# Kernel optimization log

Measured on AMD Instinct MI355X. Metric: run time of the kernel, lower is better.

Reference implementation:

```python
import jax, jax.numpy as jnp
import numpy as np

HIDDEN = 1024
HEADS = 16
HEAD_DIM = HIDDEN // HEADS
SCALE = HEAD_DIM ** -0.5


def setup_inputs() -> dict:
    key = jax.random.key(0)
    kx, kw, ko = jax.random.split(key, 3)
    x = jax.random.normal(kx, (2, 2048, HIDDEN), dtype=jnp.float32)
    # nn.Linear(hidden, 3*hidden, bias=False): weight shape [3*hidden, hidden]
    w_qkv = jax.random.normal(kw, (3 * HIDDEN, HIDDEN), dtype=jnp.float32) * (HIDDEN ** -0.5)
    w_out = jax.random.normal(ko, (HIDDEN, HIDDEN), dtype=jnp.float32) * (HIDDEN ** -0.5)
    return {"x": x, "w_qkv": w_qkv, "w_out": w_out}


def reference(x, w_qkv, w_out):
    b, s, d = x.shape
    qkv = jnp.einsum('bsd,ed->bse', x, w_qkv)  # [b,s,3d]
    q, k, v = jnp.split(qkv, 3, axis=-1)
    def heads(t):
        return t.reshape(b, s, HEADS, HEAD_DIM).transpose(0, 2, 1, 3)  # [b,h,s,hd]
    q, k, v = heads(q), heads(k), heads(v)
    scores = jnp.einsum('bhqd,bhkd->bhqk', q, k) * SCALE
    attn = jax.nn.softmax(scores, axis=-1)
    out = jnp.einsum('bhqk,bhkd->bhqd', attn, v)
    out = out.transpose(0, 2, 1, 3).reshape(b, s, d)
    return jnp.einsum('bsd,ed->bse', out, w_out)
```

## Files before the change

### kernel.cpp

```cpp
#include <hip/hip_runtime.h>
#include <hip/hip_bf16.h>
#include <stdint.h>

typedef __bf16 bf16;
typedef __bf16 bf16x8 __attribute__((ext_vector_type(8)));
typedef float f32x4 __attribute__((ext_vector_type(4)));

#define HIDDEN 1024
#define HEADS  16
#define HD     64
#define SEQ    2048
#define BATCH  2
#define NTOK   (BATCH*SEQ)
#define E3     (3*HIDDEN)

#define QSCALE (0.125f * 1.44269504088896f)

#if __has_builtin(__builtin_amdgcn_exp2f)
#define EXP2(x) __builtin_amdgcn_exp2f(x)
#else
#define EXP2(x) __expf((x) * 0.69314718055995f)
#endif

static __device__ __forceinline__ uint32_t pkbf(float a, float b) {
  union { bf16 h[2]; uint32_t u; } x;
  x.h[0] = (bf16)a; x.h[1] = (bf16)b;
  return x.u;
}

__global__ __launch_bounds__(256) void k_convert(
    const float* __restrict__ x, const float* __restrict__ wqkv, const float* __restrict__ wout,
    bf16* __restrict__ xb, bf16* __restrict__ wqkvb, bf16* __restrict__ woutb)
{
  const int NX = NTOK*HIDDEN/4, NW = E3*HIDDEN/4;
  int i = blockIdx.x*256 + threadIdx.x;
  const float4* s; bf16* d; int o;
  if (i < NX)            { s=(const float4*)x;    d=xb;    o=i; }
  else if (i < NX+NW)    { s=(const float4*)wqkv; d=wqkvb; o=i-NX; }
  else                   { s=(const float4*)wout; d=woutb; o=i-NX-NW; }
  float4 v = s[o];
  union { bf16 b[4]; uint2 u; } p;
  p.b[0]=(bf16)v.x; p.b[1]=(bf16)v.y; p.b[2]=(bf16)v.z; p.b[3]=(bf16)v.w;
  *(uint2*)(d + (size_t)o*4) = p.u;
}

template<int EPI, int BM>
__global__ __launch_bounds__(256) void k_gemm(
    const bf16* __restrict__ A, const bf16* __restrict__ B,
    bf16* __restrict__ Oq, bf16* __restrict__ Ok, bf16* __restrict__ Ov,
    float* __restrict__ Of, int M, int N, int K, int nbn)
{
  constexpr int MI = BM/32;
  __shared__ bf16 As[BM*32];
  __shared__ bf16 Bs[128*32];
  const int t = threadIdx.x;
  const int lane = t & 63;
  const int w = t >> 6;
  const int g = lane >> 4;
  const int l15 = lane & 15;
  const int wm = (w >> 1) * (BM/2), wn = (w & 1) * 64;
  const int bm = blockIdx.x / nbn, bn = blockIdx.x % nbn;
  const int brow = bm*BM, bcol = bn*128;

  f32x4 acc[MI][4];
  #pragma unroll
  for (int mi=0;mi<MI;mi++)
    #pragma unroll
    for (int ni=0;ni<4;ni++)
      #pragma unroll
      for (int r=0;r<4;r++) acc[mi][ni][r] = 0.f;

  const int nk = K >> 5;
  for (int kt = 0; kt < nk; ++kt) {
    if constexpr (BM == 128) {
      int ch = w*128 + lane;
      const bf16* ga = A + (size_t)(brow + (ch>>2))*K + kt*32 + (ch&3)*8;
      __builtin_amdgcn_global_load_lds((const uint32_t*)ga, (uint32_t*)(As + (w*128)*8), 16, 0, 0);
      int ch2 = ch + 64;
      const bf16* ga2 = A + (size_t)(brow + (ch2>>2))*K + kt*32 + (ch2&3)*8;
      __builtin_amdgcn_global_load_lds((const uint32_t*)ga2, (uint32_t*)(As + (w*128+64)*8), 16, 0, 0);
    } else {
      int ch = w*64 + lane;
      const bf16* ga = A + (size_t)(brow + (ch>>2))*K + kt*32 + (ch&3)*8;
      __builtin_amdgcn_global_load_lds((const uint32_t*)ga, (uint32_t*)(As + (w*64)*8), 16, 0, 0);
    }
    {
      int ch = w*128 + lane;
      const bf16* gb = B + (size_t)(bcol + (ch>>2))*K + kt*32 + (ch&3)*8;
      __builtin_amdgcn_global_load_lds((const uint32_t*)gb, (uint32_t*)(Bs + (w*128)*8), 16, 0, 0);
      int ch2 = ch + 64;
      const bf16* gb2 = B + (size_t)(bcol + (ch2>>2))*K + kt*32 + (ch2&3)*8;
      __builtin_amdgcn_global_load_lds((const uint32_t*)gb2, (uint32_t*)(Bs + (w*128+64)*8), 16, 0, 0);
    }
    __syncthreads();
    bf16x8 af[MI], bfr[4];
    #pragma unroll
    for (int mi=0;mi<MI;mi++) af[mi]  = *(const bf16x8*)(As + (wm + mi*16 + l15)*32 + g*8);
    #pragma unroll
    for (int ni=0;ni<4;ni++) bfr[ni] = *(const bf16x8*)(Bs + (wn + ni*16 + l15)*32 + g*8);
    #pragma unroll
    for (int mi=0;mi<MI;mi++)
      #pragma unroll
      for (int ni=0;ni<4;ni++)
        acc[mi][ni] = __builtin_amdgcn_mfma_f32_16x16x32_bf16(af[mi], bfr[ni], acc[mi][ni], 0, 0, 0);
    __syncthreads();
  }

  #pragma unroll
  for (int mi=0;mi<MI;mi++) {
    #pragma unroll
    for (int ni=0;ni<4;ni++) {
      #pragma unroll
      for (int r=0;r<4;r++) {
        float val = acc[mi][ni][r];
        int m = brow + wm + mi*16 + 4*g + r;
        int e = bcol + wn + ni*16 + l15;
        if (EPI == 0) {
          int part = e >> 10, we = e & 1023;
          int hh = we >> 6, dd = we & 63;
          int b = m >> 11, sb = m & 2047;
          size_t idx = (((size_t)b*HEADS + hh)*SEQ + sb)*HD + dd;
          if (part == 0)      Oq[idx] = (bf16)(val * QSCALE);
          else if (part == 1) Ok[idx] = (bf16)val;
          else                Ov[idx] = (bf16)val;
        } else {
          Of[(size_t)m*HIDDEN + e] = val;
        }
      }
    }
  }
}

__global__ __launch_bounds__(256, 2) void k_attn(
    const bf16* __restrict__ Qg, const bf16* __restrict__ Kg, const bf16* __restrict__ Vg,
    bf16* __restrict__ Og)
{
  __shared__ bf16 Kl[64*64];
  __shared__ bf16 Vt[64*64];
  const int t = threadIdx.x;
  const int lane = t & 63;
  const int w = t >> 6;
  const int g = lane >> 4;
  const int q = lane & 15;
  const int bh = blockIdx.x >> 4;
  const int qb = blockIdx.x & 15;
  const int q0 = qb*128 + w*32;
  const size_t bhS = (size_t)bh * SEQ * HD;

  bf16x8 qf[2][2];
  #pragma unroll
  for (int qs=0;qs<2;qs++) {
    const bf16* qrow = Qg + bhS + (size_t)(q0 + 16*qs + q)*HD + 8*g;
    qf[qs][0] = *(const bf16x8*)(qrow);
    qf[qs][1] = *(const bf16x8*)(qrow + 32);
  }

  f32x4 ot[2][4];
  #pragma unroll
  for (int qs=0;qs<2;qs++)
    #pragma unroll
    for (int df=0;df<4;df++)
      #pragma unroll
      for (int r=0;r<4;r++) ot[qs][df][r] = 0.f;
  float mrun0 = -3.0e38f, mrun1 = -3.0e38f, lrun0 = 0.f, lrun1 = 0.f;

  const int kr0 = t >> 3, kp0 = t & 7;
  const int kv0 = (t & 31)*2;
  const int dd0 = (t >> 5)*8;
  const int kvf0 = kv0 >> 4, gv = (kv0 >> 2) & 3, rv = kv0 & 3;
  const int pos0 = 32*(kvf0 >> 1) + 8*gv + 4*(kvf0 & 1) + rv;

  auto loadK = [&](int it, uint4& a, uint4& b) {
    const bf16* p0 = Kg + bhS + (size_t)(it*64 + kr0)*HD + kp0*8;
    a = *(const uint4*)p0;
    b = *(const uint4*)(p0 + 32*HD);
  };
  auto writeK = [&](uint4 a, uint4 b) {
    int sw = (kp0 ^ (kr0 & 7)) * 16;
    *(uint4*)((char*)Kl + kr0*128 + sw) = a;
    *(uint4*)((char*)Kl + (kr0+32)*128 + sw) = b;
  };
  auto loadV = [&](int it, uint4& a, uint4& b) {
    const bf16* vg = Vg + bhS + (size_t)(it*64 + kv0)*HD + dd0;
    a = *(const uint4*)vg;
    b = *(const uint4*)(vg + HD);
  };
  auto writeVt = [&](uint4 va, uint4 vb) {
    const uint32_t* pa = (const uint32_t*)&va;
    const uint32_t* pb = (const uint32_t*)&vb;
    #pragma unroll
    for (int jj=0;jj<8;jj++) {
      int dd = dd0 + jj;
      uint32_t pr = __builtin_amdgcn_perm(pb[jj>>1], pa[jj>>1],
                                          (jj&1) ? 0x07060302u : 0x05040100u);
      int byte = (dd*128 + pos0*2) ^ (jj<<4);
      *(uint32_t*)((char*)Vt + byte) = pr;
    }
  };

  uint4 ka, kb, va, vb;
  loadK(0, ka, kb);
  loadV(0, va, vb);

  const int NT = SEQ/64;
  for (int it = 0; it < NT; ++it) {
    __syncthreads();
    writeK(ka, kb);
    writeVt(va, vb);
    __syncthreads();
    if (it+1 < NT) {
      loadK(it+1, ka, kb);
      loadV(it+1, va, vb);
    }

    f32x4 sf[2][4];
    #pragma unroll
    for (int qs=0;qs<2;qs++)
      #pragma unroll
      for (int kvf=0;kvf<4;kvf++)
        #pragma unroll
        for (int r=0;r<4;r++) sf[qs][kvf][r] = 0.f;
    #pragma unroll
    for (int kvf=0;kvf<4;kvf++) {
      int row = 16*kvf + q;
      #pragma unroll
      for (int kc=0;kc<2;kc++) {
        int byte = row*128 + ((16*g + 64*kc) ^ ((row&7)<<4));
        bf16x8 kf = *(const bf16x8*)((const char*)Kl + byte);
        sf[0][kvf] = __builtin_amdgcn_mfma_f32_16x16x32_bf16(kf, qf[0][kc], sf[0][kvf], 0,0,0);
        sf[1][kvf] = __builtin_amdgcn_mfma_f32_16x16x32_bf16(kf, qf[1][kc], sf[1][kvf], 0,0,0);
      }
    }

    float pm0 = -3.0e38f, pm1 = -3.0e38f;
    #pragma unroll
    for (int kvf=0;kvf<4;kvf++)
      #pragma unroll
      for (int r=0;r<4;r++) {
        pm0 = fmaxf(pm0, sf[0][kvf][r]);
        pm1 = fmaxf(pm1, sf[1][kvf][r]);
      }
    pm0 = fmaxf(pm0, __shfl_xor(pm0, 16, 64));
    pm0 = fmaxf(pm0, __shfl_xor(pm0, 32, 64));
    pm1 = fmaxf(pm1, __shfl_xor(pm1, 16, 64));
    pm1 = fmaxf(pm1, __shfl_xor(pm1, 32, 64));

    bool need = (pm0 - mrun0 > 8.f) || (pm1 - mrun1 > 8.f);
    if (__any(need)) {
      float mn0 = fmaxf(mrun0, pm0), mn1 = fmaxf(mrun1, pm1);
      float a0 = EXP2(mrun0 - mn0), a1 = EXP2(mrun1 - mn1);
      lrun0 *= a0; lrun1 *= a1;
      #pragma unroll
      for (int df=0;df<4;df++)
        #pragma unroll
        for (int r=0;r<4;r++) { ot[0][df][r] *= a0; ot[1][df][r] *= a1; }
      mrun0 = mn0; mrun1 = mn1;
    }
    float rs0 = 0.f, rs1 = 0.f;
    #pragma unroll
    for (int kvf=0;kvf<4;kvf++)
      #pragma unroll
      for (int r=0;r<4;r++) {
        float p0 = EXP2(sf[0][kvf][r] - mrun0); sf[0][kvf][r] = p0; rs0 += p0;
        float p1 = EXP2(sf[1][kvf][r] - mrun1); sf[1][kvf][r] = p1; rs1 += p1;
      }
    rs0 += __shfl_xor(rs0, 16, 64); rs0 += __shfl_xor(rs0, 32, 64);
    rs1 += __shfl_xor(rs1, 16, 64); rs1 += __shfl_xor(rs1, 32, 64);
    lrun0 += rs0; lrun1 += rs1;

    uint32_t pk[2][4][2];
    #pragma unroll
    for (int qs=0;qs<2;qs++)
      #pragma unroll
      for (int kvf=0;kvf<4;kvf++) {
        pk[qs][kvf][0] = pkbf(sf[qs][kvf][0], sf[qs][kvf][1]);
        pk[qs][kvf][1] = pkbf(sf[qs][kvf][2], sf[qs][kvf][3]);
      }

    #pragma unroll
    for (int kc=0;kc<2;kc++) {
      union { uint32_t u[4]; bf16x8 v; } pf0, pf1;
      pf0.u[0] = pk[0][2*kc][0]; pf0.u[1] = pk[0][2*kc][1];
      pf0.u[2] = pk[0][2*kc+1][0]; pf0.u[3] = pk[0][2*kc+1][1];
      pf1.u[0] = pk[1][2*kc][0]; pf1.u[1] = pk[1][2*kc][1];
      pf1.u[2] = pk[1][2*kc+1][0]; pf1.u[3] = pk[1][2*kc+1][1];
      #pragma unroll
      for (int df=0;df<4;df++) {
        int row = 16*df + q;
        int byte = row*128 + ((16*g + 64*kc) ^ ((row&7)<<4));
        bf16x8 vf = *(const bf16x8*)((const char*)Vt + byte);
        ot[0][df] = __builtin_amdgcn_mfma_f32_16x16x32_bf16(vf, pf0.v, ot[0][df], 0,0,0);
        ot[1][df] = __builtin_amdgcn_mfma_f32_16x16x32_bf16(vf, pf1.v, ot[1][df], 0,0,0);
      }
    }
  }

  float inv0 = 1.0f / lrun0, inv1 = 1.0f / lrun1;
  int b = bh >> 4, head = bh & 15;
  #pragma unroll
  for (int qs=0;qs<2;qs++) {
    float inv = qs ? inv1 : inv0;
    size_t orow = ((size_t)b*SEQ + q0 + 16*qs + q)*HIDDEN + head*HD;
    #pragma unroll
    for (int df=0;df<4;df++) {
      uint2 pr;
      pr.x = pkbf(ot[qs][df][0]*inv, ot[qs][df][1]*inv);
      pr.y = pkbf(ot[qs][df][2]*inv, ot[qs][df][3]*inv);
      *(uint2*)(Og + orow + 16*df + 4*g) = pr;
    }
  }
}

extern "C" void kernel_launch(void* const* d_in, const int* in_sizes, int n_in,
                              void* d_out, int out_size, void* d_ws, size_t ws_size,
                              hipStream_t stream)
{
  (void)in_sizes; (void)n_in; (void)out_size; (void)ws_size;
  const float* x    = (const float*)d_in[0];
  const float* wqkv = (const float*)d_in[1];
  const float* wout = (const float*)d_in[2];
  float* out = (float*)d_out;
  char* ws = (char*)d_ws;
  bf16* xb    = (bf16*)(ws);
  bf16* wqkvb = (bf16*)(ws + 8388608);
  bf16* woutb = (bf16*)(ws + 14680064);
  bf16* Q     = (bf16*)(ws + 16777216);
  bf16* K     = (bf16*)(ws + 25165824);
  bf16* V     = (bf16*)(ws + 33554432);
  bf16* O     = (bf16*)(ws + 41943040);

  k_convert<<<8192, 256, 0, stream>>>(x, wqkv, wout, xb, wqkvb, woutb);
  k_gemm<0,128><<<32*24, 256, 0, stream>>>(xb, wqkvb, Q, K, V, nullptr, NTOK, E3, HIDDEN, 24);
  k_attn<<<512, 256, 0, stream>>>(Q, K, V, O);
  k_gemm<1,64><<<64*8, 256, 0, stream>>>(O, woutb, nullptr, nullptr, nullptr, out, NTOK, HIDDEN, HIDDEN, 8);
}
```

Baseline: 194.9 us.

## Double-buffer attention K/V tiles with software-pipelined QK/softmax-PV and widen GEMM K-tile

The GEMM now loads 64-wide K slices per iteration into swizzled shared memory, which halves the number of barrier pairs and is meant to avoid LDS bank conflicts. The attention kernel double-buffers its K and V tiles. It interleaves the QK^T of the next tile with the softmax and PV of the previous one, and raises wave priority around the MFMA blocks. This should overlap matrix-core work with softmax math and LDS traffic. The cost is double the LDS footprint and more live registers, which may lower occupancy under launch_bounds(256,2).

```diff
diff --git a/kernel.cpp b/kernel.cpp
--- a/kernel.cpp
+++ b/kernel.cpp
@@ -51,8 +51,8 @@
     float* __restrict__ Of, int M, int N, int K, int nbn)
 {
   constexpr int MI = BM/32;
-  __shared__ bf16 As[BM*32];
-  __shared__ bf16 Bs[128*32];
+  __shared__ bf16 As[BM*64];
+  __shared__ bf16 Bs[128*64];
   const int t = threadIdx.x;
   const int lane = t & 63;
   const int w = t >> 6;
@@ -70,39 +70,44 @@
       #pragma unroll
       for (int r=0;r<4;r++) acc[mi][ni][r] = 0.f;
 
-  const int nk = K >> 5;
+  const int nk = K >> 6;
   for (int kt = 0; kt < nk; ++kt) {
-    if constexpr (BM == 128) {
-      int ch = w*128 + lane;
-      const bf16* ga = A + (size_t)(brow + (ch>>2))*K + kt*32 + (ch&3)*8;
-      __builtin_amdgcn_global_load_lds((const uint32_t*)ga, (uint32_t*)(As + (w*128)*8), 16, 0, 0);
-      int ch2 = ch + 64;
-      const bf16* ga2 = A + (size_t)(brow + (ch2>>2))*K + kt*32 + (ch2&3)*8;
-      __builtin_amdgcn_global_load_lds((const uint32_t*)ga2, (uint32_t*)(As + (w*128+64)*8), 16, 0, 0);
-    } else {
-      int ch = w*64 + lane;
-      const bf16* ga = A + (size_t)(brow + (ch>>2))*K + kt*32 + (ch&3)*8;
-      __builtin_amdgcn_global_load_lds((const uint32_t*)ga, (uint32_t*)(As + (w*64)*8), 16, 0, 0);
-    }
-    {
-      int ch = w*128 + lane;
-      const bf16* gb = B + (size_t)(bcol + (ch>>2))*K + kt*32 + (ch&3)*8;
-      __builtin_amdgcn_global_load_lds((const uint32_t*)gb, (uint32_t*)(Bs + (w*128)*8), 16, 0, 0);
-      int ch2 = ch + 64;
-      const bf16* gb2 = B + (size_t)(bcol + (ch2>>2))*K + kt*32 + (ch2&3)*8;
-      __builtin_amdgcn_global_load_lds((const uint32_t*)gb2, (uint32_t*)(Bs + (w*128+64)*8), 16, 0, 0);
+    #pragma unroll
+    for (int j=0; j<BM/32; j++) {
+      int ch = w*(BM*2) + j*64 + lane;
+      int row = ch>>3, part = ch&7;
+      const bf16* ga = A + (size_t)(brow+row)*K + kt*64 + (part ^ (row&7))*8;
+      __builtin_amdgcn_global_load_lds((const uint32_t*)ga,
+          (uint32_t*)(As + (size_t)(w*(BM*2) + j*64)*8), 16, 0, 0);
+    }
+    #pragma unroll
+    for (int j=0; j<4; j++) {
+      int ch = w*256 + j*64 + lane;
+      int row = ch>>3, part = ch&7;
+      const bf16* gb = B + (size_t)(bcol+row)*K + kt*64 + (part ^ (row&7))*8;
+      __builtin_amdgcn_global_load_lds((const uint32_t*)gb,
+          (uint32_t*)(Bs + (size_t)(w*256 + j*64)*8), 16, 0, 0);
     }
     __syncthreads();
-    bf16x8 af[MI], bfr[4];
-    #pragma unroll
-    for (int mi=0;mi<MI;mi++) af[mi]  = *(const bf16x8*)(As + (wm + mi*16 + l15)*32 + g*8);
-    #pragma unroll
-    for (int ni=0;ni<4;ni++) bfr[ni] = *(const bf16x8*)(Bs + (wn + ni*16 + l15)*32 + g*8);
-    #pragma unroll
-    for (int mi=0;mi<MI;mi++)
-      #pragma unroll
-      for (int ni=0;ni<4;ni++)
-        acc[mi][ni] = __builtin_amdgcn_mfma_f32_16x16x32_bf16(af[mi], bfr[ni], acc[mi][ni], 0, 0, 0);
+    #pragma unroll
+    for (int kc=0; kc<2; kc++) {
+      bf16x8 af[MI], bfr[4];
+      #pragma unroll
+      for (int mi=0;mi<MI;mi++) {
+        int row = wm + mi*16 + l15;
+        af[mi] = *(const bf16x8*)((const char*)As + row*128 + ((kc*64 + g*16) ^ ((row&7)<<4)));
+      }
+      #pragma unroll
+      for (int ni=0;ni<4;ni++) {
+        int row = wn + ni*16 + l15;
+        bfr[ni] = *(const bf16x8*)((const char*)Bs + row*128 + ((kc*64 + g*16) ^ ((row&7)<<4)));
+      }
+      #pragma unroll
+      for (int mi=0;mi<MI;mi++)
+        #pragma unroll
+        for (int ni=0;ni<4;ni++)
+          acc[mi][ni] = __builtin_amdgcn_mfma_f32_16x16x32_bf16(af[mi], bfr[ni], acc[mi][ni], 0, 0, 0);
+    }
     __syncthreads();
   }
 
@@ -135,8 +140,8 @@
     const bf16* __restrict__ Qg, const bf16* __restrict__ Kg, const bf16* __restrict__ Vg,
     bf16* __restrict__ Og)
 {
-  __shared__ bf16 Kl[64*64];
-  __shared__ bf16 Vt[64*64];
+  __shared__ bf16 Kl[2][64*64];
+  __shared__ bf16 Vt[2][64*64];
   const int t = threadIdx.x;
   const int lane = t & 63;
   const int w = t >> 6;
@@ -175,63 +180,54 @@
     a = *(const uint4*)p0;
     b = *(const uint4*)(p0 + 32*HD);
   };
-  auto writeK = [&](uint4 a, uint4 b) {
+  auto writeK = [&](int buf, uint4 a, uint4 b) {
     int sw = (kp0 ^ (kr0 & 7)) * 16;
-    *(uint4*)((char*)Kl + kr0*128 + sw) = a;
-    *(uint4*)((char*)Kl + (kr0+32)*128 + sw) = b;
+    char* base = (char*)&Kl[buf][0];
+    *(uint4*)(base + kr0*128 + sw) = a;
+    *(uint4*)(base + (kr0+32)*128 + sw) = b;
   };
   auto loadV = [&](int it, uint4& a, uint4& b) {
     const bf16* vg = Vg + bhS + (size_t)(it*64 + kv0)*HD + dd0;
     a = *(const uint4*)vg;
     b = *(const uint4*)(vg + HD);
   };
-  auto writeVt = [&](uint4 va, uint4 vb) {
+  auto writeVt = [&](int buf, uint4 va, uint4 vb) {
     const uint32_t* pa = (const uint32_t*)&va;
     const uint32_t* pb = (const uint32_t*)&vb;
+    char* base = (char*)&Vt[buf][0];
     #pragma unroll
     for (int jj=0;jj<8;jj++) {
       int dd = dd0 + jj;
       uint32_t pr = __builtin_amdgcn_perm(pb[jj>>1], pa[jj>>1],
                                           (jj&1) ? 0x07060302u : 0x05040100u);
       int byte = (dd*128 + pos0*2) ^ (jj<<4);
-      *(uint32_t*)((char*)Vt + byte) = pr;
-    }
-  };
-
-  uint4 ka, kb, va, vb;
-  loadK(0, ka, kb);
-  loadV(0, va, vb);
-
-  const int NT = SEQ/64;
-  for (int it = 0; it < NT; ++it) {
-    __syncthreads();
-    writeK(ka, kb);
-    writeVt(va, vb);
-    __syncthreads();
-    if (it+1 < NT) {
-      loadK(it+1, ka, kb);
-      loadV(it+1, va, vb);
-    }
-
-    f32x4 sf[2][4];
+      *(uint32_t*)(base + byte) = pr;
+    }
+  };
+
+  auto doQK = [&](const char* Kbase, f32x4 (&sf)[2][4]) {
     #pragma unroll
     for (int qs=0;qs<2;qs++)
       #pragma unroll
       for (int kvf=0;kvf<4;kvf++)
         #pragma unroll
         for (int r=0;r<4;r++) sf[qs][kvf][r] = 0.f;
+    __builtin_amdgcn_s_setprio(1);
     #pragma unroll
     for (int kvf=0;kvf<4;kvf++) {
       int row = 16*kvf + q;
       #pragma unroll
       for (int kc=0;kc<2;kc++) {
         int byte = row*128 + ((16*g + 64*kc) ^ ((row&7)<<4));
-        bf16x8 kf = *(const bf16x8*)((const char*)Kl + byte);
+        bf16x8 kf = *(const bf16x8*)(Kbase + byte);
         sf[0][kvf] = __builtin_amdgcn_mfma_f32_16x16x32_bf16(kf, qf[0][kc], sf[0][kvf], 0,0,0);
         sf[1][kvf] = __builtin_amdgcn_mfma_f32_16x16x32_bf16(kf, qf[1][kc], sf[1][kvf], 0,0,0);
       }
     }
-
+    __builtin_amdgcn_s_setprio(0);
+  };
+
+  auto doSMPV = [&](const char* Vbase, f32x4 (&sf)[2][4]) {
     float pm0 = -3.0e38f, pm1 = -3.0e38f;
     #pragma unroll
     for (int kvf=0;kvf<4;kvf++)
@@ -277,6 +273,7 @@
         pk[qs][kvf][1] = pkbf(sf[qs][kvf][2], sf[qs][kvf][3]);
       }
 
+    __builtin_amdgcn_s_setprio(1);
     #pragma unroll
     for (int kc=0;kc<2;kc++) {
       union { uint32_t u[4]; bf16x8 v; } pf0, pf1;
@@ -288,12 +285,44 @@
       for (int df=0;df<4;df++) {
         int row = 16*df + q;
         int byte = row*128 + ((16*g + 64*kc) ^ ((row&7)<<4));
-        bf16x8 vf = *(const bf16x8*)((const char*)Vt + byte);
+        bf16x8 vf = *(const bf16x8*)(Vbase + byte);
         ot[0][df] = __builtin_amdgcn_mfma_f32_16x16x32_bf16(vf, pf0.v, ot[0][df], 0,0,0);
         ot[1][df] = __builtin_amdgcn_mfma_f32_16x16x32_bf16(vf, pf1.v, ot[1][df], 0,0,0);
       }
     }
-  }
+    __builtin_amdgcn_s_setprio(0);
+  };
+
+  const char* K0 = (const char*)&Kl[0][0];
+  const char* K1 = (const char*)&Kl[1][0];
+  const char* V0 = (const char*)&Vt[0][0];
+  const char* V1 = (const char*)&Vt[1][0];
+
+  uint4 ka, kb, va, vb;
+  loadK(0, ka, kb); loadV(0, va, vb);
+  writeK(0, ka, kb); writeVt(0, va, vb);
+  __syncthreads();
+  loadK(1, ka, kb); loadV(1, va, vb);
+
+  f32x4 sfA[2][4], sfB[2][4];
+  const int NT = SEQ/64;
+  for (int it = 0; it < NT; it += 2) {
+    doQK(K0, sfA);
+    if (it > 0) doSMPV(V1, sfB);
+    __syncthreads();
+    writeK(1, ka, kb); writeVt(1, va, vb);
+    __syncthreads();
+    if (it + 2 < NT) { loadK(it+2, ka, kb); loadV(it+2, va, vb); }
+    doQK(K1, sfB);
+    doSMPV(V0, sfA);
+    if (it + 2 < NT) {
+      __syncthreads();
+      writeK(0, ka, kb); writeVt(0, va, vb);
+      __syncthreads();
+      if (it + 3 < NT) { loadK(it+3, ka, kb); loadV(it+3, va, vb); }
+    }
+  }
+  doSMPV(V1, sfB);
 
   float inv0 = 1.0f / lrun0, inv1 = 1.0f / lrun1;
   int b = bh >> 4, head = bh & 15;
```

After: 180.3 us. 7.5% less time.

## Double-buffer GEMM LDS tiles and stream attention K directly from global

Applied to the files above, without the earlier changes.

The GEMM now stages A/B tiles into two LDS buffers, prefetching the next k-tile while computing the current one. The attention kernel drops the K LDS staging and loads K fragments directly from global memory into registers. It double-buffers the transposed V tile with a two-ahead register prefetch and a single barrier per iteration. It also raises wave priority around the MFMA blocks. The aim is to hide load latency and cut barriers, at the cost of more LDS and of exposed global latency on the K loads.

```diff
diff --git a/kernel.cpp b/kernel.cpp
--- a/kernel.cpp
+++ b/kernel.cpp
@@ -51,8 +51,8 @@
     float* __restrict__ Of, int M, int N, int K, int nbn)
 {
   constexpr int MI = BM/32;
-  __shared__ bf16 As[BM*32];
-  __shared__ bf16 Bs[128*32];
+  __shared__ bf16 As[2][BM*32];
+  __shared__ bf16 Bs[2][128*32];
   const int t = threadIdx.x;
   const int lane = t & 63;
   const int w = t >> 6;
@@ -70,34 +70,41 @@
       #pragma unroll
       for (int r=0;r<4;r++) acc[mi][ni][r] = 0.f;
 
-  const int nk = K >> 5;
-  for (int kt = 0; kt < nk; ++kt) {
+  auto stage = [&](int kt, int buf) {
     if constexpr (BM == 128) {
-      int ch = w*128 + lane;
-      const bf16* ga = A + (size_t)(brow + (ch>>2))*K + kt*32 + (ch&3)*8;
-      __builtin_amdgcn_global_load_lds((const uint32_t*)ga, (uint32_t*)(As + (w*128)*8), 16, 0, 0);
-      int ch2 = ch + 64;
-      const bf16* ga2 = A + (size_t)(brow + (ch2>>2))*K + kt*32 + (ch2&3)*8;
-      __builtin_amdgcn_global_load_lds((const uint32_t*)ga2, (uint32_t*)(As + (w*128+64)*8), 16, 0, 0);
+      #pragma unroll
+      for (int j=0;j<2;j++) {
+        int ch = w*128 + j*64 + lane;
+        const bf16* ga = A + (size_t)(brow + (ch>>2))*K + kt*32 + (ch&3)*8;
+        __builtin_amdgcn_global_load_lds((const uint32_t*)ga,
+            (uint32_t*)(&As[buf][0] + (size_t)(w*128 + j*64)*8), 16, 0, 0);
+      }
     } else {
       int ch = w*64 + lane;
       const bf16* ga = A + (size_t)(brow + (ch>>2))*K + kt*32 + (ch&3)*8;
-      __builtin_amdgcn_global_load_lds((const uint32_t*)ga, (uint32_t*)(As + (w*64)*8), 16, 0, 0);
-    }
-    {
-      int ch = w*128 + lane;
+      __builtin_amdgcn_global_load_lds((const uint32_t*)ga,
+          (uint32_t*)(&As[buf][0] + (size_t)(w*64)*8), 16, 0, 0);
+    }
+    #pragma unroll
+    for (int j=0;j<2;j++) {
+      int ch = w*128 + j*64 + lane;
       const bf16* gb = B + (size_t)(bcol + (ch>>2))*K + kt*32 + (ch&3)*8;
-      __builtin_amdgcn_global_load_lds((const uint32_t*)gb, (uint32_t*)(Bs + (w*128)*8), 16, 0, 0);
-      int ch2 = ch + 64;
-      const bf16* gb2 = B + (size_t)(bcol + (ch2>>2))*K + kt*32 + (ch2&3)*8;
-      __builtin_amdgcn_global_load_lds((const uint32_t*)gb2, (uint32_t*)(Bs + (w*128+64)*8), 16, 0, 0);
-    }
-    __syncthreads();
+      __builtin_amdgcn_global_load_lds((const uint32_t*)gb,
+          (uint32_t*)(&Bs[buf][0] + (size_t)(w*128 + j*64)*8), 16, 0, 0);
+    }
+  };
+
+  const int nk = K >> 5;
+  stage(0, 0);
+  __syncthreads();
+  for (int kt = 0; kt < nk; ++kt) {
+    int cur = kt & 1;
+    if (kt+1 < nk) stage(kt+1, cur^1);
     bf16x8 af[MI], bfr[4];
     #pragma unroll
-    for (int mi=0;mi<MI;mi++) af[mi]  = *(const bf16x8*)(As + (wm + mi*16 + l15)*32 + g*8);
-    #pragma unroll
-    for (int ni=0;ni<4;ni++) bfr[ni] = *(const bf16x8*)(Bs + (wn + ni*16 + l15)*32 + g*8);
+    for (int mi=0;mi<MI;mi++) af[mi]  = *(const bf16x8*)(&As[cur][0] + (wm + mi*16 + l15)*32 + g*8);
+    #pragma unroll
+    for (int ni=0;ni<4;ni++) bfr[ni] = *(const bf16x8*)(&Bs[cur][0] + (wn + ni*16 + l15)*32 + g*8);
     #pragma unroll
     for (int mi=0;mi<MI;mi++)
       #pragma unroll
@@ -135,8 +142,7 @@
     const bf16* __restrict__ Qg, const bf16* __restrict__ Kg, const bf16* __restrict__ Vg,
     bf16* __restrict__ Og)
 {
-  __shared__ bf16 Kl[64*64];
-  __shared__ bf16 Vt[64*64];
+  __shared__ bf16 Vt[2][64*64];
   const int t = threadIdx.x;
   const int lane = t & 63;
   const int w = t >> 6;
@@ -164,55 +170,49 @@
       for (int r=0;r<4;r++) ot[qs][df][r] = 0.f;
   float mrun0 = -3.0e38f, mrun1 = -3.0e38f, lrun0 = 0.f, lrun1 = 0.f;
 
-  const int kr0 = t >> 3, kp0 = t & 7;
   const int kv0 = (t & 31)*2;
   const int dd0 = (t >> 5)*8;
   const int kvf0 = kv0 >> 4, gv = (kv0 >> 2) & 3, rv = kv0 & 3;
   const int pos0 = 32*(kvf0 >> 1) + 8*gv + 4*(kvf0 & 1) + rv;
 
-  auto loadK = [&](int it, uint4& a, uint4& b) {
-    const bf16* p0 = Kg + bhS + (size_t)(it*64 + kr0)*HD + kp0*8;
-    a = *(const uint4*)p0;
-    b = *(const uint4*)(p0 + 32*HD);
-  };
-  auto writeK = [&](uint4 a, uint4 b) {
-    int sw = (kp0 ^ (kr0 & 7)) * 16;
-    *(uint4*)((char*)Kl + kr0*128 + sw) = a;
-    *(uint4*)((char*)Kl + (kr0+32)*128 + sw) = b;
-  };
   auto loadV = [&](int it, uint4& a, uint4& b) {
     const bf16* vg = Vg + bhS + (size_t)(it*64 + kv0)*HD + dd0;
     a = *(const uint4*)vg;
     b = *(const uint4*)(vg + HD);
   };
-  auto writeVt = [&](uint4 va, uint4 vb) {
+  auto writeVt = [&](int buf, uint4 va, uint4 vb) {
     const uint32_t* pa = (const uint32_t*)&va;
     const uint32_t* pb = (const uint32_t*)&vb;
+    char* base = (char*)&Vt[buf][0];
     #pragma unroll
     for (int jj=0;jj<8;jj++) {
       int dd = dd0 + jj;
       uint32_t pr = __builtin_amdgcn_perm(pb[jj>>1], pa[jj>>1],
                                           (jj&1) ? 0x07060302u : 0x05040100u);
       int byte = (dd*128 + pos0*2) ^ (jj<<4);
-      *(uint32_t*)((char*)Vt + byte) = pr;
+      *(uint32_t*)(base + byte) = pr;
     }
   };
 
-  uint4 ka, kb, va, vb;
-  loadK(0, ka, kb);
+  uint4 va, vb;
   loadV(0, va, vb);
+  writeVt(0, va, vb);
+  __syncthreads();
+  loadV(1, va, vb);
 
   const int NT = SEQ/64;
   for (int it = 0; it < NT; ++it) {
-    __syncthreads();
-    writeK(ka, kb);
-    writeVt(va, vb);
-    __syncthreads();
-    if (it+1 < NT) {
-      loadK(it+1, ka, kb);
-      loadV(it+1, va, vb);
-    }
-
+    const int cur = it & 1;
+
+    bf16x8 kf[4][2];
+    {
+      const bf16* kbase = Kg + bhS + (size_t)(it*64 + q)*HD + 8*g;
+      #pragma unroll
+      for (int kvf=0;kvf<4;kvf++) {
+        kf[kvf][0] = *(const bf16x8*)(kbase + (size_t)(16*kvf)*HD);
+        kf[kvf][1] = *(const bf16x8*)(kbase + (size_t)(16*kvf)*HD + 32);
+      }
+    }
     f32x4 sf[2][4];
     #pragma unroll
     for (int qs=0;qs<2;qs++)
@@ -220,17 +220,15 @@
       for (int kvf=0;kvf<4;kvf++)
         #pragma unroll
         for (int r=0;r<4;r++) sf[qs][kvf][r] = 0.f;
-    #pragma unroll
-    for (int kvf=0;kvf<4;kvf++) {
-      int row = 16*kvf + q;
+    __builtin_amdgcn_s_setprio(1);
+    #pragma unroll
+    for (int kvf=0;kvf<4;kvf++)
       #pragma unroll
       for (int kc=0;kc<2;kc++) {
-        int byte = row*128 + ((16*g + 64*kc) ^ ((row&7)<<4));
-        bf16x8 kf = *(const bf16x8*)((const char*)Kl + byte);
-        sf[0][kvf] = __builtin_amdgcn_mfma_f32_16x16x32_bf16(kf, qf[0][kc], sf[0][kvf], 0,0,0);
-        sf[1][kvf] = __builtin_amdgcn_mfma_f32_16x16x32_bf16(kf, qf[1][kc], sf[1][kvf], 0,0,0);
-      }
-    }
+        sf[0][kvf] = __builtin_amdgcn_mfma_f32_16x16x32_bf16(kf[kvf][kc], qf[0][kc], sf[0][kvf], 0,0,0);
+        sf[1][kvf] = __builtin_amdgcn_mfma_f32_16x16x32_bf16(kf[kvf][kc], qf[1][kc], sf[1][kvf], 0,0,0);
+      }
+    __builtin_amdgcn_s_setprio(0);
 
     float pm0 = -3.0e38f, pm1 = -3.0e38f;
     #pragma unroll
@@ -277,6 +275,7 @@
         pk[qs][kvf][1] = pkbf(sf[qs][kvf][2], sf[qs][kvf][3]);
       }
 
+    __builtin_amdgcn_s_setprio(1);
     #pragma unroll
     for (int kc=0;kc<2;kc++) {
       union { uint32_t u[4]; bf16x8 v; } pf0, pf1;
@@ -288,11 +287,16 @@
       for (int df=0;df<4;df++) {
         int row = 16*df + q;
         int byte = row*128 + ((16*g + 64*kc) ^ ((row&7)<<4));
-        bf16x8 vf = *(const bf16x8*)((const char*)Vt + byte);
+        bf16x8 vf = *(const bf16x8*)((const char*)&Vt[cur][0] + byte);
         ot[0][df] = __builtin_amdgcn_mfma_f32_16x16x32_bf16(vf, pf0.v, ot[0][df], 0,0,0);
         ot[1][df] = __builtin_amdgcn_mfma_f32_16x16x32_bf16(vf, pf1.v, ot[1][df], 0,0,0);
       }
     }
+    __builtin_amdgcn_s_setprio(0);
+
+    if (it+1 < NT) writeVt(cur^1, va, vb);
+    if (it+2 < NT) loadV(it+2, va, vb);
+    __syncthreads();
   }
 
   float inv0 = 1.0f / lrun0, inv1 = 1.0f / lrun1;
```

New measurement: 208.2 us. +6.8%, slower.
